# Optimization experiments

Measured on AMD Instinct MI355X. Metric: run time of the kernel, lower is better.

## Reference

```python
import jax, jax.numpy as jnp
import numpy as np

B, N, C, H = 4, 2048, 1024, 16
D = C // H
SCALE = D ** -0.5


def setup_inputs() -> dict:
    key = jax.random.key(0)
    k1, k2, k3 = jax.random.split(key, 3)
    x = jax.random.normal(k1, (B, N, C), dtype=jnp.float32)
    w_qkv = jax.random.normal(k2, (C, 3 * C), dtype=jnp.float32) * (C ** -0.5)
    w_proj = jax.random.normal(k3, (C, C), dtype=jnp.float32) * (C ** -0.5)
    b_proj = jnp.zeros((C,), dtype=jnp.float32)
    return {"x": x, "w_qkv": w_qkv, "w_proj": w_proj, "b_proj": b_proj}


def reference(x, w_qkv, w_proj, b_proj):
    # qkv projection (no bias): [B,N,3C] -> [3,B,H,N,D]
    qkv = (x @ w_qkv).reshape(B, N, 3, H, D).transpose(2, 0, 3, 1, 4)
    q, k, v = qkv[0], qkv[1], qkv[2]
    # scores [B,H,N,N]
    attn = jax.nn.softmax(jnp.einsum('bhnd,bhmd->bhnm', q, k) * SCALE, axis=-1)
    out = jnp.einsum('bhnm,bhmd->bhnd', attn, v)          # [B,H,N,D]
    out = out.transpose(0, 2, 1, 3).reshape(B, N, C)       # [B,N,C]
    return out @ w_proj + b_proj
```

## Files before the change

### kernel.cpp

```cpp
#include <hip/hip_runtime.h>
#include <hip/hip_bf16.h>
#include <cstdint>
#include <cstddef>

typedef unsigned int uint;
typedef unsigned short ushort;

constexpr int Bn = 4, Nn = 2048, Cc = 1024, Hh = 16;
constexpr int ROWS = Bn * Nn;
constexpr int QKVC = 3 * Cc;
constexpr float SCALE = 0.125f;
constexpr float SL2 = 0.18033688011118f;

typedef __bf16 bf16_t;
typedef bf16_t bf16x8 __attribute__((ext_vector_type(8)));
typedef float f32x4 __attribute__((ext_vector_type(4)));

__device__ __forceinline__ ushort f2bf(float f) {
  union { __bf16 b; ushort u; } cv;
  cv.b = (__bf16)f;
  return cv.u;
}
__device__ __forceinline__ float exp2v(float x) { return __builtin_exp2f(x); }

__device__ __forceinline__ void gload_lds16(const void* g, void* l) {
  __builtin_amdgcn_global_load_lds(
      (const __attribute__((address_space(1))) void*)g,
      (__attribute__((address_space(3))) void*)l, 16, 0, 0);
}

__global__ __launch_bounds__(256) void cvt_bf16_kernel(
    const float* __restrict__ in, ushort* __restrict__ out) {
  int i = blockIdx.x * 256 + threadIdx.x;
  const float4* ip = (const float4*)in;
  float4 a = ip[i * 2], b = ip[i * 2 + 1];
  uint4 w;
  w.x = (uint)f2bf(a.x) | ((uint)f2bf(a.y) << 16);
  w.y = (uint)f2bf(a.z) | ((uint)f2bf(a.w) << 16);
  w.z = (uint)f2bf(b.x) | ((uint)f2bf(b.y) << 16);
  w.w = (uint)f2bf(b.z) | ((uint)f2bf(b.w) << 16);
  ((uint4*)out)[i] = w;
}

__global__ __launch_bounds__(256) void transpose_cvt_kernel(
    const float* __restrict__ W, ushort* __restrict__ Wt, int K, int N) {
  __shared__ float tile[64][65];
  const int n0 = blockIdx.x * 64, k0 = blockIdx.y * 64;
  const int tid = threadIdx.x;
#pragma unroll
  for (int it = 0; it < 16; it++) {
    int idx = tid + it * 256;
    int r = idx >> 6, c = idx & 63;
    tile[r][c] = W[(size_t)(k0 + r) * N + n0 + c];
  }
  __syncthreads();
#pragma unroll
  for (int it = 0; it < 16; it++) {
    int idx = tid + it * 256;
    int r = idx >> 6, c = idx & 63;
    Wt[(size_t)(n0 + r) * K + k0 + c] = f2bf(tile[c][r]);
  }
}

template <int MODE>
__global__ __launch_bounds__(256) void gemm128_kernel(
    const ushort* __restrict__ A, const ushort* __restrict__ Bt,
    void* __restrict__ Cout, void* __restrict__ Vout,
    const float* __restrict__ bias, int M, int N, int K) {
  __shared__ ushort As[128 * 32];
  __shared__ ushort Bs[128 * 32];
  const int tid = threadIdx.x;
  const int lane = tid & 63;
  const int wid = tid >> 6;
  const int wm = wid >> 1, wn = wid & 1;
  const int l16 = lane & 15, g = lane >> 4;
  const int n0 = blockIdx.x * 128, m0 = blockIdx.y * 128;

  const int c0 = tid, c1 = tid + 256;
  const ushort* Ab = A + (size_t)m0 * K;
  const ushort* Bb = Bt + (size_t)n0 * K;
  f32x4 acc[4][4] = {};

  for (int k0 = 0; k0 < K; k0 += 32) {
    gload_lds16(Ab + (size_t)(c0 >> 2) * K + k0 + (c0 & 3) * 8, As + c0 * 8);
    gload_lds16(Ab + (size_t)(c1 >> 2) * K + k0 + (c1 & 3) * 8, As + c1 * 8);
    gload_lds16(Bb + (size_t)(c0 >> 2) * K + k0 + (c0 & 3) * 8, Bs + c0 * 8);
    gload_lds16(Bb + (size_t)(c1 >> 2) * K + k0 + (c1 & 3) * 8, Bs + c1 * 8);
    __syncthreads();
    bf16x8 af[4], bfr[4];
#pragma unroll
    for (int mf = 0; mf < 4; mf++)
      af[mf] = *(const bf16x8*)(As + (wm * 64 + mf * 16 + l16) * 32 + g * 8);
#pragma unroll
    for (int nf = 0; nf < 4; nf++)
      bfr[nf] = *(const bf16x8*)(Bs + (wn * 64 + nf * 16 + l16) * 32 + g * 8);
#pragma unroll
    for (int mf = 0; mf < 4; mf++)
#pragma unroll
      for (int nf = 0; nf < 4; nf++)
        acc[mf][nf] = __builtin_amdgcn_mfma_f32_16x16x32_bf16(af[mf], bfr[nf], acc[mf][nf], 0, 0, 0);
    __syncthreads();
  }

#pragma unroll
  for (int mf = 0; mf < 4; mf++) {
    const int orow0 = m0 + wm * 64 + mf * 16 + g * 4;
#pragma unroll
    for (int nf = 0; nf < 4; nf++) {
      int col = n0 + wn * 64 + nf * 16 + l16;
      if (MODE == 0) {
        if (col < 2048) {
#pragma unroll
          for (int r = 0; r < 4; r++)
            ((ushort*)Cout)[(size_t)(orow0 + r) * 2048 + col] = f2bf(acc[mf][nf][r]);
        } else {
          int hh = (col - 2048) >> 6, dd = (col - 2048) & 63;
          int bb = orow0 >> 11, nn = orow0 & 2047;
          ushort4 w;
          w.x = f2bf(acc[mf][nf][0]); w.y = f2bf(acc[mf][nf][1]);
          w.z = f2bf(acc[mf][nf][2]); w.w = f2bf(acc[mf][nf][3]);
          *(ushort4*)((ushort*)Vout + ((size_t)(bb * 16 + hh) * 64 + dd) * 2048 + nn) = w;
        }
      } else {
#pragma unroll
        for (int r = 0; r < 4; r++)
          ((float*)Cout)[(size_t)(orow0 + r) * N + col] = acc[mf][nf][r] + bias[col];
      }
    }
  }
}

__global__ __launch_bounds__(256, 4) void flash_mfma_kernel(
    const ushort* __restrict__ qk, const ushort* __restrict__ vt,
    ushort* __restrict__ obf) {
  __shared__ ushort Ks[2][64 * 64];
  __shared__ ushort Vs[64 * 64];
  __shared__ ushort Ps[4 * 32 * 64];
  const int tid = threadIdx.x;
  const int lane = tid & 63, wid = tid >> 6;
  const int l16 = lane & 15, g = lane >> 4;
  const int bh = blockIdx.y, b = bh >> 4, h = bh & 15;
  const int q0 = blockIdx.x * 128 + wid * 32;
  ushort* Pw = Ps + wid * (32 * 64);

  const int sc0 = tid, sc1 = tid + 256;
  const int sr0 = sc0 >> 3, scol0 = ((sc0 & 7) ^ (sr0 & 7)) * 8;
  const int sr1 = sc1 >> 3, scol1 = ((sc1 & 7) ^ (sr1 & 7)) * 8;
  const ushort* Kbase = qk + (size_t)b * Nn * 2048 + 1024 + h * 64;
  const ushort* Vbase = vt + (size_t)bh * 64 * 2048;

#define KSTAGE(buf, kv0)                                                      \
  do {                                                                        \
    gload_lds16(Kbase + (size_t)((kv0) + sr0) * 2048 + scol0,                 \
                &Ks[buf][0] + sc0 * 8);                                       \
    gload_lds16(Kbase + (size_t)((kv0) + sr1) * 2048 + scol1,                 \
                &Ks[buf][0] + sc1 * 8);                                       \
  } while (0)
#define VSTAGE(kv0)                                                           \
  do {                                                                        \
    gload_lds16(Vbase + (size_t)sr0 * 2048 + (kv0) + scol0, Vs + sc0 * 8);    \
    gload_lds16(Vbase + (size_t)sr1 * 2048 + (kv0) + scol1, Vs + sc1 * 8);    \
  } while (0)

  bf16x8 qf[2][2];
#pragma unroll
  for (int qh = 0; qh < 2; qh++)
#pragma unroll
    for (int kc = 0; kc < 2; kc++)
      qf[qh][kc] = *(const bf16x8*)(
          qk + (size_t)(b * Nn + q0 + qh * 16 + l16) * 2048 + h * 64 + kc * 32 + g * 8);

  f32x4 oacc[2][4] = {};
  float mrun[2] = {-INFINITY, -INFINITY};
  float lrun[2] = {0.f, 0.f};

  KSTAGE(0, 0);

  for (int t = 0; t < Nn / 64; ++t) {
    const int cur = t & 1;
    VSTAGE(t * 64);
    if (t < Nn / 64 - 1) {
      KSTAGE(cur ^ 1, (t + 1) * 64);
      asm volatile("s_waitcnt vmcnt(4)" ::: "memory");
    } else {
      asm volatile("s_waitcnt vmcnt(2)" ::: "memory");
    }
    __builtin_amdgcn_s_barrier();
    asm volatile("" ::: "memory");

    const ushort* Kc = &Ks[cur][0];
    f32x4 sacc[2][4] = {};
    __builtin_amdgcn_s_setprio(1);
#pragma unroll
    for (int kc = 0; kc < 2; kc++) {
#pragma unroll
      for (int jc = 0; jc < 4; jc++) {
        int row = jc * 16 + l16;
        bf16x8 kf = *(const bf16x8*)(Kc + row * 64 + ((kc * 32 + g * 8) ^ ((row & 7) << 3)));
        sacc[0][jc] = __builtin_amdgcn_mfma_f32_16x16x32_bf16(kf, qf[0][kc], sacc[0][jc], 0, 0, 0);
        sacc[1][jc] = __builtin_amdgcn_mfma_f32_16x16x32_bf16(kf, qf[1][kc], sacc[1][jc], 0, 0, 0);
      }
    }
    __builtin_amdgcn_s_setprio(0);

    float pmax[2];
#pragma unroll
    for (int qh = 0; qh < 2; qh++) {
      float mx = sacc[qh][0][0];
#pragma unroll
      for (int jc = 0; jc < 4; jc++)
#pragma unroll
        for (int r = 0; r < 4; r++) mx = fmaxf(mx, sacc[qh][jc][r]);
      mx = fmaxf(mx, __shfl_xor(mx, 16));
      mx = fmaxf(mx, __shfl_xor(mx, 32));
      pmax[qh] = mx * SL2;
    }
    bool need = (pmax[0] > mrun[0] + 8.f) || (pmax[1] > mrun[1] + 8.f);
    if (__any(need)) {
#pragma unroll
      for (int qh = 0; qh < 2; qh++) {
        float mnew = fmaxf(mrun[qh], pmax[qh]);
        float alpha = exp2v(mrun[qh] - mnew);
        mrun[qh] = mnew;
        lrun[qh] *= alpha;
#pragma unroll
        for (int r = 0; r < 4; r++) {
          float ar = __shfl(alpha, g * 4 + r);
#pragma unroll
          for (int dc = 0; dc < 4; dc++) oacc[qh][dc][r] *= ar;
        }
      }
    }
#pragma unroll
    for (int qh = 0; qh < 2; qh++) {
      int qp = qh * 16 + l16;
      float psum = 0.f;
#pragma unroll
      for (int jc = 0; jc < 4; jc++) {
        float p0 = exp2v(fmaf(sacc[qh][jc][0], SL2, -mrun[qh]));
        float p1 = exp2v(fmaf(sacc[qh][jc][1], SL2, -mrun[qh]));
        float p2 = exp2v(fmaf(sacc[qh][jc][2], SL2, -mrun[qh]));
        float p3 = exp2v(fmaf(sacc[qh][jc][3], SL2, -mrun[qh]));
        psum += (p0 + p1) + (p2 + p3);
        ushort4 pw;
        pw.x = f2bf(p0); pw.y = f2bf(p1); pw.z = f2bf(p2); pw.w = f2bf(p3);
        *(ushort4*)(Pw + qp * 64 + ((jc * 16 + g * 4) ^ ((qp & 7) << 3))) = pw;
      }
      psum += __shfl_xor(psum, 16);
      psum += __shfl_xor(psum, 32);
      lrun[qh] += psum;
    }

    if (t < Nn / 64 - 1) asm volatile("s_waitcnt vmcnt(2)" ::: "memory");
    else                 asm volatile("s_waitcnt vmcnt(0)" ::: "memory");
    __builtin_amdgcn_s_barrier();
    asm volatile("" ::: "memory");

    __builtin_amdgcn_s_setprio(1);
#pragma unroll
    for (int kc = 0; kc < 2; kc++) {
      bf16x8 pf0 = *(const bf16x8*)(Pw + l16 * 64 + ((kc * 32 + g * 8) ^ ((l16 & 7) << 3)));
      bf16x8 pf1 = *(const bf16x8*)(Pw + (16 + l16) * 64 + ((kc * 32 + g * 8) ^ ((l16 & 7) << 3)));
#pragma unroll
      for (int dc = 0; dc < 4; dc++) {
        int row = dc * 16 + l16;
        bf16x8 vf = *(const bf16x8*)(Vs + row * 64 + ((kc * 32 + g * 8) ^ ((row & 7) << 3)));
        oacc[0][dc] = __builtin_amdgcn_mfma_f32_16x16x32_bf16(pf0, vf, oacc[0][dc], 0, 0, 0);
        oacc[1][dc] = __builtin_amdgcn_mfma_f32_16x16x32_bf16(pf1, vf, oacc[1][dc], 0, 0, 0);
      }
    }
    __builtin_amdgcn_s_setprio(0);

    if (t < Nn / 64 - 1) {
      asm volatile("" ::: "memory");
      __builtin_amdgcn_s_barrier();
      asm volatile("" ::: "memory");
    }
  }
#undef KSTAGE
#undef VSTAGE

#pragma unroll
  for (int qh = 0; qh < 2; qh++) {
    float linv = 1.f / lrun[qh];
#pragma unroll
    for (int r = 0; r < 4; r++) {
      float sc = __shfl(linv, g * 4 + r);
      int grow = b * Nn + q0 + qh * 16 + g * 4 + r;
      ushort* op = obf + (size_t)grow * Cc + h * 64 + l16;
#pragma unroll
      for (int dc = 0; dc < 4; dc++)
        op[dc * 16] = f2bf(oacc[qh][dc][r] * sc);
    }
  }
}

extern "C" void kernel_launch(void* const* d_in, const int* in_sizes, int n_in,
                              void* d_out, int out_size, void* d_ws, size_t ws_size,
                              hipStream_t stream) {
  const float* x      = (const float*)d_in[0];
  const float* w_qkv  = (const float*)d_in[1];
  const float* w_proj = (const float*)d_in[2];
  const float* b_proj = (const float*)d_in[3];
  float* out = (float*)d_out;

  char* ws = (char*)d_ws;
  ushort* Xbf    = (ushort*)(ws);
  ushort* WqkvT  = (ushort*)(ws + (16u << 20));
  ushort* WprojT = (ushort*)(ws + (22u << 20));
  ushort* QKbf   = (ushort*)(ws + (24u << 20));
  ushort* Vtg    = (ushort*)(ws + (56u << 20));
  ushort* Obf    = (ushort*)(ws + (72u << 20));

  cvt_bf16_kernel<<<4096, 256, 0, stream>>>(x, Xbf);
  transpose_cvt_kernel<<<dim3(QKVC / 64, Cc / 64), 256, 0, stream>>>(w_qkv, WqkvT, Cc, QKVC);
  transpose_cvt_kernel<<<dim3(Cc / 64, Cc / 64), 256, 0, stream>>>(w_proj, WprojT, Cc, Cc);
  gemm128_kernel<0><<<dim3(QKVC / 128, ROWS / 128), 256, 0, stream>>>(
      Xbf, WqkvT, QKbf, Vtg, nullptr, ROWS, QKVC, Cc);
  flash_mfma_kernel<<<dim3(Nn / 128, Bn * Hh), 256, 0, stream>>>(QKbf, Vtg, Obf);
  gemm128_kernel<1><<<dim3(Cc / 128, ROWS / 128), 256, 0, stream>>>(
      Obf, WprojT, out, nullptr, b_proj, ROWS, Cc, Cc);
}
```

Measured before the change: 243.8 us.

## Keep softmax probabilities in registers via permlane swaps, double-buffer V, compute rowsum with MFMA

The P tile is no longer written to and read back from LDS. It is packed to bf16 with v_cvt_pk_bf16_f32 and rearranged into MFMA A-operand layout with permlane32/16 swaps. V is now double-buffered together with K, so each iteration needs a single barrier instead of three. The softmax row sum is accumulated by an extra MFMA against a ones vector rather than by shuffles. This removes LDS traffic and barriers from the attention core, at the cost of extra MFMA work and a full vmcnt(0) wait at the top of each iteration.

```diff
diff --git a/kernel.cpp b/kernel.cpp
--- a/kernel.cpp
+++ b/kernel.cpp
@@ -9,7 +9,6 @@
 constexpr int Bn = 4, Nn = 2048, Cc = 1024, Hh = 16;
 constexpr int ROWS = Bn * Nn;
 constexpr int QKVC = 3 * Cc;
-constexpr float SCALE = 0.125f;
 constexpr float SL2 = 0.18033688011118f;
 
 typedef __bf16 bf16_t;
@@ -134,14 +133,12 @@
     const ushort* __restrict__ qk, const ushort* __restrict__ vt,
     ushort* __restrict__ obf) {
   __shared__ ushort Ks[2][64 * 64];
-  __shared__ ushort Vs[64 * 64];
-  __shared__ ushort Ps[4 * 32 * 64];
+  __shared__ ushort Vs[2][64 * 64];
   const int tid = threadIdx.x;
   const int lane = tid & 63, wid = tid >> 6;
   const int l16 = lane & 15, g = lane >> 4;
   const int bh = blockIdx.y, b = bh >> 4, h = bh & 15;
   const int q0 = blockIdx.x * 128 + wid * 32;
-  ushort* Pw = Ps + wid * (32 * 64);
 
   const int sc0 = tid, sc1 = tid + 256;
   const int sr0 = sc0 >> 3, scol0 = ((sc0 & 7) ^ (sr0 & 7)) * 8;
@@ -149,17 +146,16 @@
   const ushort* Kbase = qk + (size_t)b * Nn * 2048 + 1024 + h * 64;
   const ushort* Vbase = vt + (size_t)bh * 64 * 2048;
 
-#define KSTAGE(buf, kv0)                                                      \
+#define STAGE(buf, kv0)                                                       \
   do {                                                                        \
     gload_lds16(Kbase + (size_t)((kv0) + sr0) * 2048 + scol0,                 \
                 &Ks[buf][0] + sc0 * 8);                                       \
     gload_lds16(Kbase + (size_t)((kv0) + sr1) * 2048 + scol1,                 \
                 &Ks[buf][0] + sc1 * 8);                                       \
-  } while (0)
-#define VSTAGE(kv0)                                                           \
-  do {                                                                        \
-    gload_lds16(Vbase + (size_t)sr0 * 2048 + (kv0) + scol0, Vs + sc0 * 8);    \
-    gload_lds16(Vbase + (size_t)sr1 * 2048 + (kv0) + scol1, Vs + sc1 * 8);    \
+    gload_lds16(Vbase + (size_t)sr0 * 2048 + (kv0) + scol0,                   \
+                &Vs[buf][0] + sc0 * 8);                                       \
+    gload_lds16(Vbase + (size_t)sr1 * 2048 + (kv0) + scol1,                   \
+                &Vs[buf][0] + sc1 * 8);                                       \
   } while (0)
 
   bf16x8 qf[2][2];
@@ -170,25 +166,27 @@
       qf[qh][kc] = *(const bf16x8*)(
           qk + (size_t)(b * Nn + q0 + qh * 16 + l16) * 2048 + h * 64 + kc * 32 + g * 8);
 
+  union { ushort us[8]; bf16x8 v; } onesu;
+#pragma unroll
+  for (int j = 0; j < 8; j++) onesu.us[j] = 0x3F80;
+  const bf16x8 ones = onesu.v;
+
   f32x4 oacc[2][4] = {};
+  f32x4 lacc[2] = {};
   float mrun[2] = {-INFINITY, -INFINITY};
-  float lrun[2] = {0.f, 0.f};
-
-  KSTAGE(0, 0);
+
+  STAGE(0, 0);
 
   for (int t = 0; t < Nn / 64; ++t) {
     const int cur = t & 1;
-    VSTAGE(t * 64);
-    if (t < Nn / 64 - 1) {
-      KSTAGE(cur ^ 1, (t + 1) * 64);
-      asm volatile("s_waitcnt vmcnt(4)" ::: "memory");
-    } else {
-      asm volatile("s_waitcnt vmcnt(2)" ::: "memory");
-    }
+    asm volatile("s_waitcnt vmcnt(0)" ::: "memory");
     __builtin_amdgcn_s_barrier();
     asm volatile("" ::: "memory");
+    if (t < Nn / 64 - 1) STAGE(cur ^ 1, (t + 1) * 64);
 
     const ushort* Kc = &Ks[cur][0];
+    const ushort* Vc = &Vs[cur][0];
+
     f32x4 sacc[2][4] = {};
     __builtin_amdgcn_s_setprio(1);
 #pragma unroll
@@ -206,11 +204,11 @@
     float pmax[2];
 #pragma unroll
     for (int qh = 0; qh < 2; qh++) {
-      float mx = sacc[qh][0][0];
-#pragma unroll
-      for (int jc = 0; jc < 4; jc++)
-#pragma unroll
-        for (int r = 0; r < 4; r++) mx = fmaxf(mx, sacc[qh][jc][r]);
+      float mj0 = fmaxf(fmaxf(fmaxf(sacc[qh][0][0], sacc[qh][0][1]), sacc[qh][0][2]), sacc[qh][0][3]);
+      float mj1 = fmaxf(fmaxf(fmaxf(sacc[qh][1][0], sacc[qh][1][1]), sacc[qh][1][2]), sacc[qh][1][3]);
+      float mj2 = fmaxf(fmaxf(fmaxf(sacc[qh][2][0], sacc[qh][2][1]), sacc[qh][2][2]), sacc[qh][2][3]);
+      float mj3 = fmaxf(fmaxf(fmaxf(sacc[qh][3][0], sacc[qh][3][1]), sacc[qh][3][2]), sacc[qh][3][3]);
+      float mx = fmaxf(fmaxf(fmaxf(mj0, mj1), mj2), mj3);
       mx = fmaxf(mx, __shfl_xor(mx, 16));
       mx = fmaxf(mx, __shfl_xor(mx, 32));
       pmax[qh] = mx * SL2;
@@ -222,75 +220,72 @@
         float mnew = fmaxf(mrun[qh], pmax[qh]);
         float alpha = exp2v(mrun[qh] - mnew);
         mrun[qh] = mnew;
-        lrun[qh] *= alpha;
 #pragma unroll
         for (int r = 0; r < 4; r++) {
           float ar = __shfl(alpha, g * 4 + r);
 #pragma unroll
           for (int dc = 0; dc < 4; dc++) oacc[qh][dc][r] *= ar;
+          lacc[qh][r] *= ar;
         }
       }
     }
+
+    bf16x8 pa[2][2];
 #pragma unroll
     for (int qh = 0; qh < 2; qh++) {
-      int qp = qh * 16 + l16;
-      float psum = 0.f;
+      uint pk_[4][2];
 #pragma unroll
       for (int jc = 0; jc < 4; jc++) {
         float p0 = exp2v(fmaf(sacc[qh][jc][0], SL2, -mrun[qh]));
         float p1 = exp2v(fmaf(sacc[qh][jc][1], SL2, -mrun[qh]));
         float p2 = exp2v(fmaf(sacc[qh][jc][2], SL2, -mrun[qh]));
         float p3 = exp2v(fmaf(sacc[qh][jc][3], SL2, -mrun[qh]));
-        psum += (p0 + p1) + (p2 + p3);
-        ushort4 pw;
-        pw.x = f2bf(p0); pw.y = f2bf(p1); pw.z = f2bf(p2); pw.w = f2bf(p3);
-        *(ushort4*)(Pw + qp * 64 + ((jc * 16 + g * 4) ^ ((qp & 7) << 3))) = pw;
-      }
-      psum += __shfl_xor(psum, 16);
-      psum += __shfl_xor(psum, 32);
-      lrun[qh] += psum;
-    }
-
-    if (t < Nn / 64 - 1) asm volatile("s_waitcnt vmcnt(2)" ::: "memory");
-    else                 asm volatile("s_waitcnt vmcnt(0)" ::: "memory");
-    __builtin_amdgcn_s_barrier();
-    asm volatile("" ::: "memory");
+        asm("v_cvt_pk_bf16_f32 %0, %1, %2" : "=v"(pk_[jc][0]) : "v"(p0), "v"(p1));
+        asm("v_cvt_pk_bf16_f32 %0, %1, %2" : "=v"(pk_[jc][1]) : "v"(p2), "v"(p3));
+      }
+#pragma unroll
+      for (int kc = 0; kc < 2; kc++) {
+        uint a0 = pk_[kc * 2][0], b0 = pk_[kc * 2 + 1][0];
+        asm("v_permlane32_swap_b32 %0, %1" : "+v"(a0), "+v"(b0));
+        asm("v_permlane16_swap_b32 %0, %1" : "+v"(a0), "+v"(b0));
+        uint a1 = pk_[kc * 2][1], b1 = pk_[kc * 2 + 1][1];
+        asm("v_permlane32_swap_b32 %0, %1" : "+v"(a1), "+v"(b1));
+        asm("v_permlane16_swap_b32 %0, %1" : "+v"(a1), "+v"(b1));
+        union { uint4 u; bf16x8 v; } cv;
+        cv.u.x = a0; cv.u.y = a1; cv.u.z = b0; cv.u.w = b1;
+        pa[qh][kc] = cv.v;
+      }
+    }
 
     __builtin_amdgcn_s_setprio(1);
 #pragma unroll
     for (int kc = 0; kc < 2; kc++) {
-      bf16x8 pf0 = *(const bf16x8*)(Pw + l16 * 64 + ((kc * 32 + g * 8) ^ ((l16 & 7) << 3)));
-      bf16x8 pf1 = *(const bf16x8*)(Pw + (16 + l16) * 64 + ((kc * 32 + g * 8) ^ ((l16 & 7) << 3)));
 #pragma unroll
       for (int dc = 0; dc < 4; dc++) {
         int row = dc * 16 + l16;
-        bf16x8 vf = *(const bf16x8*)(Vs + row * 64 + ((kc * 32 + g * 8) ^ ((row & 7) << 3)));
-        oacc[0][dc] = __builtin_amdgcn_mfma_f32_16x16x32_bf16(pf0, vf, oacc[0][dc], 0, 0, 0);
-        oacc[1][dc] = __builtin_amdgcn_mfma_f32_16x16x32_bf16(pf1, vf, oacc[1][dc], 0, 0, 0);
-      }
+        bf16x8 vf = *(const bf16x8*)(Vc + row * 64 + ((kc * 32 + g * 8) ^ ((row & 7) << 3)));
+        oacc[0][dc] = __builtin_amdgcn_mfma_f32_16x16x32_bf16(pa[0][kc], vf, oacc[0][dc], 0, 0, 0);
+        oacc[1][dc] = __builtin_amdgcn_mfma_f32_16x16x32_bf16(pa[1][kc], vf, oacc[1][dc], 0, 0, 0);
+      }
+      lacc[0] = __builtin_amdgcn_mfma_f32_16x16x32_bf16(pa[0][kc], ones, lacc[0], 0, 0, 0);
+      lacc[1] = __builtin_amdgcn_mfma_f32_16x16x32_bf16(pa[1][kc], ones, lacc[1], 0, 0, 0);
     }
     __builtin_amdgcn_s_setprio(0);
-
-    if (t < Nn / 64 - 1) {
-      asm volatile("" ::: "memory");
-      __builtin_amdgcn_s_barrier();
-      asm volatile("" ::: "memory");
-    }
-  }
-#undef KSTAGE
-#undef VSTAGE
+  }
+#undef STAGE
 
 #pragma unroll
   for (int qh = 0; qh < 2; qh++) {
-    float linv = 1.f / lrun[qh];
+    f32x4 linv;
+#pragma unroll
+    for (int r = 0; r < 4; r++) linv[r] = 1.f / lacc[qh][r];
 #pragma unroll
     for (int r = 0; r < 4; r++) {
-      float sc = __shfl(linv, g * 4 + r);
       int grow = b * Nn + q0 + qh * 16 + g * 4 + r;
       ushort* op = obf + (size_t)grow * Cc + h * 64 + l16;
 #pragma unroll
       for (int dc = 0; dc < 4; dc++)
-        op[dc * 16] = f2bf(oacc[qh][dc][r] * sc);
+        op[dc * 16] = f2bf(oacc[qh][dc][r] * linv[r]);
     }
   }
 }
```

Result: no change. 243.4 us (-0.2%).
